# Kernel tuning notes

Hardware: AMD Instinct MI355X
Metric: run time of the kernel (lower is better)

## Reference

```python
import jax, jax.numpy as jnp
import numpy as np

HIDDEN = 64
EMBED = 16
N_AGENTS = 1024
TRACK_LEN = 8


def setup_inputs() -> dict:
    key = jax.random.key(0)
    ks = jax.random.split(key, 6)
    s = lambda fan_in: 1.0 / np.sqrt(fan_in)
    return {
        "hidden_state": jax.random.normal(ks[0], (1, N_AGENTS, HIDDEN), jnp.float32),
        "group_track": jax.random.normal(ks[1], (N_AGENTS, TRACK_LEN, 2), jnp.float32),
        "W_e": jax.random.normal(ks[2], (2, EMBED), jnp.float32) * s(2),
        "b_e": jnp.zeros((EMBED,), jnp.float32),
        "W1": jax.random.normal(ks[3], (EMBED + HIDDEN, 2 * HIDDEN), jnp.float32) * s(EMBED + HIDDEN),
        "b1": jnp.zeros((2 * HIDDEN,), jnp.float32),
        "W2": jax.random.normal(ks[4], (2 * HIDDEN, HIDDEN), jnp.float32) * s(2 * HIDDEN),
        "b2": jnp.zeros((HIDDEN,), jnp.float32),
    }


def reference(hidden_state, group_track, W_e, b_e, W1, b1, W2, b2):
    n = group_track.shape[0]
    ends = group_track[:, -1, :]                       # [N, 2] end positions
    # rel[c, j] = end_j - end_c  (relative neighbor end pos per center agent)
    rel = ends[None, :, :] - ends[:, None, :]          # [N, N, 2]
    emb = rel @ W_e + b_e                              # [N, N, E]
    h = jnp.broadcast_to(hidden_state[0][None, :, :], (n, n, hidden_state.shape[-1]))
    x = jnp.concatenate([h, emb], axis=-1)             # [N, N, E+H] (hidden first, as in torch)
    y = jax.nn.relu(x @ W1 + b1)                       # [N, N, 2H]
    z = jax.nn.relu(y @ W2 + b2)                       # [N, N, H]
    pooled = z.max(axis=1)                             # max over neighbors -> [N, H]
    return pooled[None]                                # [1, N, H]
```

## Files before the change

### kernel.cpp

```cpp
#include <hip/hip_runtime.h>


#define N_AG 1024

typedef __attribute__((ext_vector_type(8))) short short8;
typedef __attribute__((ext_vector_type(4))) float floatx4;
typedef __attribute__((ext_vector_type(4))) unsigned int uintx4;

#if defined(__has_builtin)
#if __has_builtin(__builtin_amdgcn_cvt_pk_bf16_f32)
#define HAVE_CVT_PK_BF16 1
typedef __bf16 bf16x2 __attribute__((ext_vector_type(2)));
#endif
#endif

__device__ __forceinline__ unsigned short f2bf(float f) {
  unsigned u = __builtin_bit_cast(unsigned, f);
  u += 0x7FFFu + ((u >> 16) & 1u);
  return (unsigned short)(u >> 16);
}

__device__ __forceinline__ unsigned pack2bf(float y0, float y1) {
#ifdef HAVE_CVT_PK_BF16
  bf16x2 pk = __builtin_amdgcn_cvt_pk_bf16_f32(y0, y1);
  return __builtin_bit_cast(unsigned, pk);
#else
  return (unsigned)f2bf(y0) | ((unsigned)f2bf(y1) << 16);
#endif
}

__global__ __launch_bounds__(128) void prep_all(
    const float* __restrict__ hidden,
    const float* __restrict__ track,
    const float* __restrict__ We,
    const float* __restrict__ be,
    const float* __restrict__ W1,
    const float* __restrict__ b1,
    const float* __restrict__ W2,
    unsigned short* __restrict__ Abf,
    float* __restrict__ M2f,
    unsigned short* __restrict__ W2T)
{
  int j = blockIdx.x;
  int k = threadIdx.x;
  __shared__ float hj[64];
  if (k < 64) hj[k] = hidden[j * 64 + k];
  __syncthreads();
  float e0 = track[j * 16 + 14];
  float e1 = track[j * 16 + 15];
  float m20 = 0.f, m21 = 0.f, cb = b1[k];
#pragma unroll
  for (int t = 0; t < 16; ++t) {
    float w1v = W1[(64 + t) * 128 + k];
    m20 += We[t] * w1v;
    m21 += We[16 + t] * w1v;
    cb  += be[t] * w1v;
  }
  float acc = e0 * m20 + e1 * m21 + cb;
#pragma unroll 16
  for (int t = 0; t < 64; ++t) acc += hj[t] * W1[t * 128 + k];
  Abf[j * 128 + k] = f2bf(acc);

  if (j == 0) {
    M2f[k]       = m20;
    M2f[128 + k] = m21;
  }
  if (j < 32) {
#pragma unroll
    for (int q = 0; q < 2; ++q) {
      int idx = j * 256 + q * 128 + k;
      int n = idx >> 7, c = idx & 127;
      W2T[n * 128 + c] = f2bf(W2[c * 64 + n]);
    }
  }
}

__global__ __launch_bounds__(256) void pool_main(
    const unsigned short* __restrict__ Abf,
    const float* __restrict__ M2f,
    const float* __restrict__ track,
    const unsigned short* __restrict__ W2T,
    const float* __restrict__ b2,
    float* __restrict__ out)
{
  const int i    = blockIdx.x;
  const int lane = threadIdx.x & 63;
  const int wave = threadIdx.x >> 6;
  const int m    = lane & 15;
  const int quad = lane >> 4;

  const float e0 = track[i * 16 + 14];
  const float e1 = track[i * 16 + 15];
  float u[4][8];
#pragma unroll
  for (int kk = 0; kk < 4; ++kk) {
#pragma unroll
    for (int jj = 0; jj < 8; ++jj) {
      int kidx = kk * 32 + quad * 8 + jj;
      u[kk][jj] = e0 * M2f[kidx] + e1 * M2f[128 + kidx];
    }
  }

  short8 bfrag[4][4];
#pragma unroll
  for (int t = 0; t < 4; ++t)
#pragma unroll
    for (int kk = 0; kk < 4; ++kk)
      bfrag[t][kk] = *(const short8*)(W2T + (t * 16 + m) * 128 + kk * 32 + quad * 8);

  floatx4 mx[4];
#pragma unroll
  for (int t = 0; t < 4; ++t) mx[t] = (floatx4){-3e38f, -3e38f, -3e38f, -3e38f};

  for (int jt = wave; jt < 64; jt += 4) {
    const unsigned short* Aptr = Abf + (jt * 16 + m) * 128 + quad * 8;
    uintx4 au[4];
#pragma unroll
    for (int kk = 0; kk < 4; ++kk) {
      uintx4 raw = *(const uintx4*)(Aptr + kk * 32);
#pragma unroll
      for (int p = 0; p < 4; ++p) {
        unsigned w = raw[p];
        float lo = __builtin_bit_cast(float, w << 16);
        float hi = __builtin_bit_cast(float, w & 0xFFFF0000u);
        float y0 = fmaxf(lo - u[kk][2 * p], 0.f);
        float y1 = fmaxf(hi - u[kk][2 * p + 1], 0.f);
        au[kk][p] = pack2bf(y0, y1);
      }
    }
#pragma unroll
    for (int t = 0; t < 4; ++t) {
      floatx4 acc = (floatx4){0.f, 0.f, 0.f, 0.f};
#pragma unroll
      for (int kk = 0; kk < 4; ++kk) {
        short8 af = __builtin_bit_cast(short8, au[kk]);
        acc = __builtin_amdgcn_mfma_f32_16x16x32_bf16(af, bfrag[t][kk], acc, 0, 0, 0);
      }
#pragma unroll
      for (int r = 0; r < 4; ++r) mx[t][r] = fmaxf(mx[t][r], acc[r]);
    }
  }

  float lm[4];
#pragma unroll
  for (int t = 0; t < 4; ++t) {
    lm[t] = fmaxf(fmaxf(mx[t][0], mx[t][1]), fmaxf(mx[t][2], mx[t][3]));
    lm[t] = fmaxf(lm[t], __shfl_xor(lm[t], 16, 64));
    lm[t] = fmaxf(lm[t], __shfl_xor(lm[t], 32, 64));
  }
  __shared__ float red[4][64];
  if (quad == 0) {
#pragma unroll
    for (int t = 0; t < 4; ++t) red[wave][t * 16 + m] = lm[t];
  }
  __syncthreads();
  if (threadIdx.x < 64) {
    int n = threadIdx.x;
    float v = fmaxf(fmaxf(red[0][n], red[1][n]), fmaxf(red[2][n], red[3][n]));
    v += b2[n];
    v = v > 0.f ? v : 0.f;
    out[i * 64 + n] = v;
  }
}

extern "C" void kernel_launch(void* const* d_in, const int* in_sizes, int n_in,
                              void* d_out, int out_size, void* d_ws, size_t ws_size,
                              hipStream_t stream) {
  const float* hidden = (const float*)d_in[0];
  const float* track  = (const float*)d_in[1];
  const float* We     = (const float*)d_in[2];
  const float* be     = (const float*)d_in[3];
  const float* W1     = (const float*)d_in[4];
  const float* b1     = (const float*)d_in[5];
  const float* W2     = (const float*)d_in[6];
  const float* b2     = (const float*)d_in[7];
  float* out = (float*)d_out;

  char* ws = (char*)d_ws;
  unsigned short* Abf = (unsigned short*)ws;
  float*          M2f = (float*)(ws + 262144);
  unsigned short* W2T = (unsigned short*)(ws + 263168);

  prep_all<<<N_AG, 128, 0, stream>>>(hidden, track, We, be, W1, b1, W2, Abf, M2f, W2T);
  pool_main<<<N_AG, 256, 0, stream>>>(Abf, M2f, track, W2T, b2, out);
}
```

Baseline: 114.2 us.

## Process two center agents per block and pack bf16 via truncating perm

Each block now handles two center agents, so every loaded A tile and the resident W2 fragments feed twice as many MFMAs, halving the global A traffic per agent and the grid size. The bf16 packing switches from round-to-nearest conversion to a single byte-permute truncation, which saves ALU work in the inner loop. The cost is roughly doubled register use for the u, accumulator and max arrays, which may lower occupancy. With only 512 blocks, fewer blocks are available to spread across CUs. Truncation also introduces slightly larger rounding error.

```diff
diff --git a/kernel.cpp b/kernel.cpp
--- a/kernel.cpp
+++ b/kernel.cpp
@@ -7,26 +7,15 @@
 typedef __attribute__((ext_vector_type(4))) float floatx4;
 typedef __attribute__((ext_vector_type(4))) unsigned int uintx4;
 
-#if defined(__has_builtin)
-#if __has_builtin(__builtin_amdgcn_cvt_pk_bf16_f32)
-#define HAVE_CVT_PK_BF16 1
-typedef __bf16 bf16x2 __attribute__((ext_vector_type(2)));
-#endif
-#endif
-
 __device__ __forceinline__ unsigned short f2bf(float f) {
   unsigned u = __builtin_bit_cast(unsigned, f);
   u += 0x7FFFu + ((u >> 16) & 1u);
   return (unsigned short)(u >> 16);
 }
 
-__device__ __forceinline__ unsigned pack2bf(float y0, float y1) {
-#ifdef HAVE_CVT_PK_BF16
-  bf16x2 pk = __builtin_amdgcn_cvt_pk_bf16_f32(y0, y1);
-  return __builtin_bit_cast(unsigned, pk);
-#else
-  return (unsigned)f2bf(y0) | ((unsigned)f2bf(y1) << 16);
-#endif
+__device__ __forceinline__ unsigned pack2bf_rtz(float y0, float y1) {
+  return __builtin_amdgcn_perm(__builtin_bit_cast(unsigned, y1),
+                               __builtin_bit_cast(unsigned, y0), 0x07060302u);
 }
 
 __global__ __launch_bounds__(128) void prep_all(
@@ -83,21 +72,23 @@
     const float* __restrict__ b2,
     float* __restrict__ out)
 {
-  const int i    = blockIdx.x;
+  const int i0   = blockIdx.x * 2;
   const int lane = threadIdx.x & 63;
   const int wave = threadIdx.x >> 6;
   const int m    = lane & 15;
   const int quad = lane >> 4;
 
-  const float e0 = track[i * 16 + 14];
-  const float e1 = track[i * 16 + 15];
-  float u[4][8];
+  const float a_e0 = track[i0 * 16 + 14],       a_e1 = track[i0 * 16 + 15];
+  const float b_e0 = track[(i0 + 1) * 16 + 14], b_e1 = track[(i0 + 1) * 16 + 15];
+  float u0[4][8], u1[4][8];
 #pragma unroll
   for (int kk = 0; kk < 4; ++kk) {
 #pragma unroll
     for (int jj = 0; jj < 8; ++jj) {
       int kidx = kk * 32 + quad * 8 + jj;
-      u[kk][jj] = e0 * M2f[kidx] + e1 * M2f[128 + kidx];
+      float m2a = M2f[kidx], m2b = M2f[128 + kidx];
+      u0[kk][jj] = a_e0 * m2a + a_e1 * m2b;
+      u1[kk][jj] = b_e0 * m2a + b_e1 * m2b;
     }
   }
 
@@ -108,13 +99,17 @@
     for (int kk = 0; kk < 4; ++kk)
       bfrag[t][kk] = *(const short8*)(W2T + (t * 16 + m) * 128 + kk * 32 + quad * 8);
 
-  floatx4 mx[4];
+  floatx4 mx0[4], mx1[4];
 #pragma unroll
-  for (int t = 0; t < 4; ++t) mx[t] = (floatx4){-3e38f, -3e38f, -3e38f, -3e38f};
+  for (int t = 0; t < 4; ++t) {
+    mx0[t] = (floatx4){-3e38f, -3e38f, -3e38f, -3e38f};
+    mx1[t] = (floatx4){-3e38f, -3e38f, -3e38f, -3e38f};
+  }
 
-  for (int jt = wave; jt < 64; jt += 4) {
-    const unsigned short* Aptr = Abf + (jt * 16 + m) * 128 + quad * 8;
-    uintx4 au[4];
+  const unsigned short* Aptr = Abf + (wave * 16 + m) * 128 + quad * 8;
+#pragma unroll 2
+  for (int it = 0; it < 16; ++it, Aptr += 4 * 16 * 128) {
+    uintx4 au0[4], au1[4];
 #pragma unroll
     for (int kk = 0; kk < 4; ++kk) {
       uintx4 raw = *(const uintx4*)(Aptr + kk * 32);
@@ -123,43 +118,60 @@
         unsigned w = raw[p];
         float lo = __builtin_bit_cast(float, w << 16);
         float hi = __builtin_bit_cast(float, w & 0xFFFF0000u);
-        float y0 = fmaxf(lo - u[kk][2 * p], 0.f);
-        float y1 = fmaxf(hi - u[kk][2 * p + 1], 0.f);
-        au[kk][p] = pack2bf(y0, y1);
+        float y0a = fmaxf(lo - u0[kk][2 * p], 0.f);
+        float y1a = fmaxf(hi - u0[kk][2 * p + 1], 0.f);
+        float y0b = fmaxf(lo - u1[kk][2 * p], 0.f);
+        float y1b = fmaxf(hi - u1[kk][2 * p + 1], 0.f);
+        au0[kk][p] = pack2bf_rtz(y0a, y1a);
+        au1[kk][p] = pack2bf_rtz(y0b, y1b);
       }
     }
 #pragma unroll
     for (int t = 0; t < 4; ++t) {
-      floatx4 acc = (floatx4){0.f, 0.f, 0.f, 0.f};
+      floatx4 acc0 = (floatx4){0.f, 0.f, 0.f, 0.f};
+      floatx4 acc1 = (floatx4){0.f, 0.f, 0.f, 0.f};
 #pragma unroll
       for (int kk = 0; kk < 4; ++kk) {
-        short8 af = __builtin_bit_cast(short8, au[kk]);
-        acc = __builtin_amdgcn_mfma_f32_16x16x32_bf16(af, bfrag[t][kk], acc, 0, 0, 0);
+        acc0 = __builtin_amdgcn_mfma_f32_16x16x32_bf16(
+            __builtin_bit_cast(short8, au0[kk]), bfrag[t][kk], acc0, 0, 0, 0);
+        acc1 = __builtin_amdgcn_mfma_f32_16x16x32_bf16(
+            __builtin_bit_cast(short8, au1[kk]), bfrag[t][kk], acc1, 0, 0, 0);
       }
 #pragma unroll
-      for (int r = 0; r < 4; ++r) mx[t][r] = fmaxf(mx[t][r], acc[r]);
+      for (int r = 0; r < 4; ++r) {
+        mx0[t][r] = fmaxf(mx0[t][r], acc0[r]);
+        mx1[t][r] = fmaxf(mx1[t][r], acc1[r]);
+      }
     }
   }
 
-  float lm[4];
+  float lm0[4], lm1[4];
 #pragma unroll
   for (int t = 0; t < 4; ++t) {
-    lm[t] = fmaxf(fmaxf(mx[t][0], mx[t][1]), fmaxf(mx[t][2], mx[t][3]));
-    lm[t] = fmaxf(lm[t], __shfl_xor(lm[t], 16, 64));
-    lm[t] = fmaxf(lm[t], __shfl_xor(lm[t], 32, 64));
+    lm0[t] = fmaxf(fmaxf(mx0[t][0], mx0[t][1]), fmaxf(mx0[t][2], mx0[t][3]));
+    lm0[t] = fmaxf(lm0[t], __shfl_xor(lm0[t], 16, 64));
+    lm0[t] = fmaxf(lm0[t], __shfl_xor(lm0[t], 32, 64));
+    lm1[t] = fmaxf(fmaxf(mx1[t][0], mx1[t][1]), fmaxf(mx1[t][2], mx1[t][3]));
+    lm1[t] = fmaxf(lm1[t], __shfl_xor(lm1[t], 16, 64));
+    lm1[t] = fmaxf(lm1[t], __shfl_xor(lm1[t], 32, 64));
   }
-  __shared__ float red[4][64];
+  __shared__ float red[4][2][64];
   if (quad == 0) {
 #pragma unroll
-    for (int t = 0; t < 4; ++t) red[wave][t * 16 + m] = lm[t];
+    for (int t = 0; t < 4; ++t) {
+      red[wave][0][t * 16 + m] = lm0[t];
+      red[wave][1][t * 16 + m] = lm1[t];
+    }
   }
   __syncthreads();
-  if (threadIdx.x < 64) {
-    int n = threadIdx.x;
-    float v = fmaxf(fmaxf(red[0][n], red[1][n]), fmaxf(red[2][n], red[3][n]));
+  if (threadIdx.x < 128) {
+    int a = threadIdx.x >> 6;
+    int n = threadIdx.x & 63;
+    float v = fmaxf(fmaxf(red[0][a][n], red[1][a][n]),
+                    fmaxf(red[2][a][n], red[3][a][n]));
     v += b2[n];
     v = v > 0.f ? v : 0.f;
-    out[i * 64 + n] = v;
+    out[(i0 + a) * 64 + n] = v;
   }
 }
 
@@ -182,5 +194,5 @@
   unsigned short* W2T = (unsigned short*)(ws + 263168);
 
   prep_all<<<N_AG, 128, 0, stream>>>(hidden, track, We, be, W1, b1, W2, Abf, M2f, W2T);
-  pool_main<<<N_AG, 256, 0, stream>>>(Abf, M2f, track, W2T, b2, out);
+  pool_main<<<N_AG / 2, 256, 0, stream>>>(Abf, M2f, track, W2T, b2, out);
 }
```

After: 115.3 us. About the same (+1.0%).

## Split neighbor range across four blocks per agent with a finishing max kernel

Applied to the files above, without the earlier changes.

The main pooling kernel now launches four blocks per center agent, each covering a quarter of the neighbors, and writes partial maxima that a new finish kernel reduces before adding the bias and applying ReLU. The per-agent offset vector is precomputed in the prep kernel and stored, so the main kernel loads it instead of recomputing it. The bf16 packing switches to a single byte-permute truncation, which is cheaper but rounds toward zero. The intent is more blocks in flight and shorter per-block loops, at the cost of an extra launch, a partial-result buffer and a small loss of rounding accuracy.

```diff
diff --git a/kernel.cpp b/kernel.cpp
--- a/kernel.cpp
+++ b/kernel.cpp
@@ -7,26 +7,15 @@
 typedef __attribute__((ext_vector_type(4))) float floatx4;
 typedef __attribute__((ext_vector_type(4))) unsigned int uintx4;
 
-#if defined(__has_builtin)
-#if __has_builtin(__builtin_amdgcn_cvt_pk_bf16_f32)
-#define HAVE_CVT_PK_BF16 1
-typedef __bf16 bf16x2 __attribute__((ext_vector_type(2)));
-#endif
-#endif
-
 __device__ __forceinline__ unsigned short f2bf(float f) {
   unsigned u = __builtin_bit_cast(unsigned, f);
   u += 0x7FFFu + ((u >> 16) & 1u);
   return (unsigned short)(u >> 16);
 }
 
-__device__ __forceinline__ unsigned pack2bf(float y0, float y1) {
-#ifdef HAVE_CVT_PK_BF16
-  bf16x2 pk = __builtin_amdgcn_cvt_pk_bf16_f32(y0, y1);
-  return __builtin_bit_cast(unsigned, pk);
-#else
-  return (unsigned)f2bf(y0) | ((unsigned)f2bf(y1) << 16);
-#endif
+__device__ __forceinline__ unsigned pack2bf_rtz(float y0, float y1) {
+  return __builtin_amdgcn_perm(__builtin_bit_cast(unsigned, y1),
+                               __builtin_bit_cast(unsigned, y0), 0x07060302u);
 }
 
 __global__ __launch_bounds__(128) void prep_all(
@@ -38,7 +27,7 @@
     const float* __restrict__ b1,
     const float* __restrict__ W2,
     unsigned short* __restrict__ Abf,
-    float* __restrict__ M2f,
+    float* __restrict__ Uf,
     unsigned short* __restrict__ W2T)
 {
   int j = blockIdx.x;
@@ -56,15 +45,13 @@
     m21 += We[16 + t] * w1v;
     cb  += be[t] * w1v;
   }
-  float acc = e0 * m20 + e1 * m21 + cb;
+  float uval = e0 * m20 + e1 * m21;
+  Uf[j * 128 + k] = uval;
+  float acc = uval + cb;
 #pragma unroll 16
   for (int t = 0; t < 64; ++t) acc += hj[t] * W1[t * 128 + k];
   Abf[j * 128 + k] = f2bf(acc);
 
-  if (j == 0) {
-    M2f[k]       = m20;
-    M2f[128 + k] = m21;
-  }
   if (j < 32) {
 #pragma unroll
     for (int q = 0; q < 2; ++q) {
@@ -77,28 +64,24 @@
 
 __global__ __launch_bounds__(256) void pool_main(
     const unsigned short* __restrict__ Abf,
-    const float* __restrict__ M2f,
-    const float* __restrict__ track,
+    const float* __restrict__ Uf,
     const unsigned short* __restrict__ W2T,
-    const float* __restrict__ b2,
-    float* __restrict__ out)
+    float* __restrict__ part)
 {
-  const int i    = blockIdx.x;
+  const int i    = blockIdx.x >> 2;
+  const int h    = blockIdx.x & 3;
   const int lane = threadIdx.x & 63;
   const int wave = threadIdx.x >> 6;
   const int m    = lane & 15;
   const int quad = lane >> 4;
 
-  const float e0 = track[i * 16 + 14];
-  const float e1 = track[i * 16 + 15];
   float u[4][8];
 #pragma unroll
   for (int kk = 0; kk < 4; ++kk) {
+    floatx4 ua = *(const floatx4*)(Uf + i * 128 + kk * 32 + quad * 8);
+    floatx4 ub = *(const floatx4*)(Uf + i * 128 + kk * 32 + quad * 8 + 4);
 #pragma unroll
-    for (int jj = 0; jj < 8; ++jj) {
-      int kidx = kk * 32 + quad * 8 + jj;
-      u[kk][jj] = e0 * M2f[kidx] + e1 * M2f[128 + kidx];
-    }
+    for (int jj = 0; jj < 4; ++jj) { u[kk][jj] = ua[jj]; u[kk][4 + jj] = ub[jj]; }
   }
 
   short8 bfrag[4][4];
@@ -112,8 +95,9 @@
 #pragma unroll
   for (int t = 0; t < 4; ++t) mx[t] = (floatx4){-3e38f, -3e38f, -3e38f, -3e38f};
 
-  for (int jt = wave; jt < 64; jt += 4) {
-    const unsigned short* Aptr = Abf + (jt * 16 + m) * 128 + quad * 8;
+  const unsigned short* Aptr = Abf + ((16 * h + wave) * 16 + m) * 128 + quad * 8;
+#pragma unroll 2
+  for (int s = 0; s < 4; ++s, Aptr += 4 * 16 * 128) {
     uintx4 au[4];
 #pragma unroll
     for (int kk = 0; kk < 4; ++kk) {
@@ -125,17 +109,16 @@
         float hi = __builtin_bit_cast(float, w & 0xFFFF0000u);
         float y0 = fmaxf(lo - u[kk][2 * p], 0.f);
         float y1 = fmaxf(hi - u[kk][2 * p + 1], 0.f);
-        au[kk][p] = pack2bf(y0, y1);
+        au[kk][p] = pack2bf_rtz(y0, y1);
       }
     }
 #pragma unroll
     for (int t = 0; t < 4; ++t) {
       floatx4 acc = (floatx4){0.f, 0.f, 0.f, 0.f};
 #pragma unroll
-      for (int kk = 0; kk < 4; ++kk) {
-        short8 af = __builtin_bit_cast(short8, au[kk]);
-        acc = __builtin_amdgcn_mfma_f32_16x16x32_bf16(af, bfrag[t][kk], acc, 0, 0, 0);
-      }
+      for (int kk = 0; kk < 4; ++kk)
+        acc = __builtin_amdgcn_mfma_f32_16x16x32_bf16(
+            __builtin_bit_cast(short8, au[kk]), bfrag[t][kk], acc, 0, 0, 0);
 #pragma unroll
       for (int r = 0; r < 4; ++r) mx[t][r] = fmaxf(mx[t][r], acc[r]);
     }
@@ -156,11 +139,22 @@
   __syncthreads();
   if (threadIdx.x < 64) {
     int n = threadIdx.x;
-    float v = fmaxf(fmaxf(red[0][n], red[1][n]), fmaxf(red[2][n], red[3][n]));
-    v += b2[n];
-    v = v > 0.f ? v : 0.f;
-    out[i * 64 + n] = v;
+    part[blockIdx.x * 64 + n] =
+        fmaxf(fmaxf(red[0][n], red[1][n]), fmaxf(red[2][n], red[3][n]));
   }
+}
+
+__global__ __launch_bounds__(256) void finish(
+    const float* __restrict__ part,
+    const float* __restrict__ b2,
+    float* __restrict__ out)
+{
+  int idx = blockIdx.x * 256 + threadIdx.x;
+  int i = idx >> 6, n = idx & 63;
+  float v = fmaxf(fmaxf(part[(4 * i) * 64 + n], part[(4 * i + 1) * 64 + n]),
+                  fmaxf(part[(4 * i + 2) * 64 + n], part[(4 * i + 3) * 64 + n]));
+  v += b2[n];
+  out[idx] = v > 0.f ? v : 0.f;
 }
 
 extern "C" void kernel_launch(void* const* d_in, const int* in_sizes, int n_in,
@@ -178,9 +172,11 @@
 
   char* ws = (char*)d_ws;
   unsigned short* Abf = (unsigned short*)ws;
-  float*          M2f = (float*)(ws + 262144);
-  unsigned short* W2T = (unsigned short*)(ws + 263168);
+  unsigned short* W2T = (unsigned short*)(ws + 262144);
+  float*          Uf  = (float*)(ws + 280576);
+  float*          prt = (float*)(ws + 804864);
 
-  prep_all<<<N_AG, 128, 0, stream>>>(hidden, track, We, be, W1, b1, W2, Abf, M2f, W2T);
-  pool_main<<<N_AG, 256, 0, stream>>>(Abf, M2f, track, W2T, b2, out);
+  prep_all<<<N_AG, 128, 0, stream>>>(hidden, track, We, be, W1, b1, W2, Abf, Uf, W2T);
+  pool_main<<<N_AG * 4, 256, 0, stream>>>(Abf, Uf, W2T, prt);
+  finish<<<256, 256, 0, stream>>>(prt, b2, out);
 }
```

Measured after the change: 139.7 us. +22.4%, slower.
